# Performance work log

Measured on AMD Instinct MI355X. Metric: run time of the kernel, lower is better.

## Reference

```python
import jax, jax.numpy as jnp
import numpy as np
import math

B, H, S, D = 2, 16, 2048, 128
INV_SCALE = math.sqrt(D)  # divisor applied to QK^T logits (dropout_p = 0.0)


def setup_inputs() -> dict:
    key = jax.random.key(0)
    kq, kk, kv = jax.random.split(key, 3)
    return {
        "query": jax.random.normal(kq, (B, H, S, D), dtype=jnp.float32),
        "key": jax.random.normal(kk, (B, H, S, D), dtype=jnp.float32),
        "value": jax.random.normal(kv, (B, H, S, D), dtype=jnp.float32),
    }


def reference(query, key, value):
    # v1 = Q @ K^T ; v2 = v1 / inv_scale ; v3 = softmax(v2, -1) ; dropout(p=0) is identity ; out = v3 @ V
    scores = jnp.einsum("bhqd,bhkd->bhqk", query, key) / INV_SCALE  # [B,H,Sq,Sk]
    probs = jax.nn.softmax(scores, axis=-1)
    return jnp.einsum("bhqk,bhkd->bhqd", probs, value)  # [B,H,Sq,D]
```

## Files before the change

### kernel.cpp

```cpp
#include <hip/hip_runtime.h>
#include <hip/hip_bf16.h>

typedef __bf16 bf16x8 __attribute__((ext_vector_type(8)));
typedef float f32x4 __attribute__((ext_vector_type(4)));

#define S_LEN 2048
#define D_DIM 128
#define BH 32
#define BN 64
#define NT (S_LEN / BN)
#define NWAVE 8
#define QSCALE (0.08838834764831845f * 1.4426950408889634f)


__global__ __launch_bounds__(512, 4)
void fa_fwd_kernel(const float* __restrict__ Qg, const float* __restrict__ Kg,
                   const float* __restrict__ Vg, float* __restrict__ Og) {
    __shared__ __bf16 Klds[BN][D_DIM + 8];
    __shared__ __bf16 Vlds[D_DIM][BN + 8];
    __shared__ __bf16 Plds[NWAVE][16][BN + 8];

    const int bh   = blockIdx.x & (BH - 1);
    const int qt   = blockIdx.x >> 5;
    const int tid  = threadIdx.x;
    const int wave = tid >> 6;
    const int lane = tid & 63;
    const int quad = lane >> 4;
    const int m16  = lane & 15;

    const float* Qh = Qg + bh * (S_LEN * D_DIM);
    const float* Kh = Kg + bh * (S_LEN * D_DIM);
    const float* Vh = Vg + bh * (S_LEN * D_DIM);
    float*       Oh = Og + bh * (S_LEN * D_DIM);

    const int qrow_base = qt * 128 + wave * 16;

    bf16x8 qf[4];
#pragma unroll
    for (int ks = 0; ks < 4; ++ks) {
        const float* qp = Qh + (qrow_base + m16) * D_DIM + ks * 32 + quad * 8;
        const float4 a = *(const float4*)(qp);
        const float4 b = *(const float4*)(qp + 4);
        bf16x8 f;
        f[0] = (__bf16)(a.x * QSCALE); f[1] = (__bf16)(a.y * QSCALE);
        f[2] = (__bf16)(a.z * QSCALE); f[3] = (__bf16)(a.w * QSCALE);
        f[4] = (__bf16)(b.x * QSCALE); f[5] = (__bf16)(b.y * QSCALE);
        f[6] = (__bf16)(b.z * QSCALE); f[7] = (__bf16)(b.w * QSCALE);
        qf[ks] = f;
    }

    f32x4 o_acc[8];
#pragma unroll
    for (int nt = 0; nt < 8; ++nt) {
        o_acc[nt][0] = 0.f; o_acc[nt][1] = 0.f; o_acc[nt][2] = 0.f; o_acc[nt][3] = 0.f;
    }
    float l_part[4] = {0.f, 0.f, 0.f, 0.f};

    for (int kt = 0; kt < NT; ++kt) {
        __syncthreads();

        {
            const float* kg = Kh + kt * BN * D_DIM;
#pragma unroll
            for (int i = 0; i < 2; ++i) {
                const int idx = tid + i * 512;
                const int r = idx >> 4, c8 = idx & 15;
                const float4 a = *(const float4*)(kg + r * D_DIM + c8 * 8);
                const float4 b = *(const float4*)(kg + r * D_DIM + c8 * 8 + 4);
                bf16x8 w;
                w[0] = (__bf16)a.x; w[1] = (__bf16)a.y; w[2] = (__bf16)a.z; w[3] = (__bf16)a.w;
                w[4] = (__bf16)b.x; w[5] = (__bf16)b.y; w[6] = (__bf16)b.z; w[7] = (__bf16)b.w;
                *(bf16x8*)&Klds[r][c8 * 8] = w;
            }
            const float* vg = Vh + kt * BN * D_DIM;
            const int c4 = tid & 31, rp = tid >> 5;
#pragma unroll
            for (int i = 0; i < 2; ++i) {
                const int r = (rp + i * 16) * 2;
                const float4 v0 = *(const float4*)(vg + r * D_DIM + c4 * 4);
                const float4 v1 = *(const float4*)(vg + (r + 1) * D_DIM + c4 * 4);
                const float* p0 = reinterpret_cast<const float*>(&v0);
                const float* p1 = reinterpret_cast<const float*>(&v1);
                const int kb = r >> 3, jj = r & 7;
#pragma unroll
                for (int j = 0; j < 4; ++j) {
                    const int d = c4 * 4 + j;
                    union { __bf16 h[2]; unsigned int u; } pk;
                    pk.h[0] = (__bf16)p0[j]; pk.h[1] = (__bf16)p1[j];
                    *(unsigned int*)&Vlds[d][((kb ^ ((d >> 3) & 7)) << 3) + jj] = pk.u;
                }
            }
        }
        __syncthreads();

        f32x4 sacc[4];
#pragma unroll
        for (int nt = 0; nt < 4; ++nt) {
            sacc[nt][0] = 0.f; sacc[nt][1] = 0.f; sacc[nt][2] = 0.f; sacc[nt][3] = 0.f;
        }
#pragma unroll
        for (int ks = 0; ks < 4; ++ks)
#pragma unroll
            for (int nt = 0; nt < 4; ++nt) {
                const bf16x8 kf = *(const bf16x8*)&Klds[nt * 16 + m16][ks * 32 + quad * 8];
                sacc[nt] = __builtin_amdgcn_mfma_f32_16x16x32_bf16(qf[ks], kf, sacc[nt], 0, 0, 0);
            }

#pragma unroll
        for (int nt = 0; nt < 4; ++nt)
#pragma unroll
            for (int r = 0; r < 4; ++r) {
                const float p = __builtin_amdgcn_exp2f(sacc[nt][r]);
                l_part[r] += p;
                Plds[wave][quad * 4 + r][nt * 16 + m16] = (__bf16)p;
            }

#pragma unroll
        for (int ks = 0; ks < 2; ++ks) {
            const bf16x8 pa = *(const bf16x8*)&Plds[wave][m16][ks * 32 + quad * 8];
#pragma unroll
            for (int nt = 0; nt < 8; ++nt) {
                const int d = nt * 16 + m16;
                const bf16x8 vf =
                    *(const bf16x8*)&Vlds[d][((ks * 4 + quad) ^ ((d >> 3) & 7)) << 3];
                o_acc[nt] = __builtin_amdgcn_mfma_f32_16x16x32_bf16(pa, vf, o_acc[nt], 0, 0, 0);
            }
        }
    }

#pragma unroll
    for (int xm = 1; xm <= 8; xm <<= 1)
#pragma unroll
        for (int r = 0; r < 4; ++r)
            l_part[r] += __shfl_xor(l_part[r], xm, 64);

    float inv[4];
#pragma unroll
    for (int r = 0; r < 4; ++r) inv[r] = 1.0f / l_part[r];
#pragma unroll
    for (int nt = 0; nt < 8; ++nt)
#pragma unroll
        for (int r = 0; r < 4; ++r)
            Oh[(qrow_base + quad * 4 + r) * D_DIM + nt * 16 + m16] = o_acc[nt][r] * inv[r];
}

extern "C" void kernel_launch(void* const* d_in, const int* in_sizes, int n_in,
                              void* d_out, int out_size, void* d_ws, size_t ws_size,
                              hipStream_t stream) {
    const float* Q = (const float*)d_in[0];
    const float* K = (const float*)d_in[1];
    const float* V = (const float*)d_in[2];
    float* O = (float*)d_out;
    dim3 grid(BH * (S_LEN / 128));
    fa_fwd_kernel<<<grid, 512, 0, stream>>>(Q, K, V, O);
}
```

Before: 223.0 us.

## Register-prefetch next K/V tile and restructure V transpose store with MFMA priority

Global loads of the next K and V tiles are issued into registers right after the LDS barrier, so their latency overlaps the current tile's QK and PV MFMA work. The V transpose is reorganised so each lane loads eight rows of two columns and writes two full bf16x8 vectors to LDS, replacing many 32-bit scattered stores. s_setprio raises wave priority around the MFMA blocks. The cost is extra VGPRs for the staging registers, which may pressure occupancy under the 512x4 launch bounds.

```diff
diff --git a/kernel.cpp b/kernel.cpp
--- a/kernel.cpp
+++ b/kernel.cpp
@@ -56,48 +56,71 @@
     }
     float l_part[4] = {0.f, 0.f, 0.f, 0.f};
 
+    const int krow = tid >> 4;
+    const int kc8  = tid & 15;
+    const int vd0   = lane * 2;
+    const int vrow  = wave * 8;
+    const int vslot = (wave ^ ((vd0 >> 3) & 7)) << 3;
+
+    float4 kreg[4];
+    float2 vreg[8];
+    {
+        const float* kg = Kh;
+        kreg[0] = *(const float4*)(kg + krow * D_DIM + kc8 * 8);
+        kreg[1] = *(const float4*)(kg + krow * D_DIM + kc8 * 8 + 4);
+        kreg[2] = *(const float4*)(kg + (32 + krow) * D_DIM + kc8 * 8);
+        kreg[3] = *(const float4*)(kg + (32 + krow) * D_DIM + kc8 * 8 + 4);
+        const float* vp = Vh + vrow * D_DIM + vd0;
+#pragma unroll
+        for (int kr = 0; kr < 8; ++kr)
+            vreg[kr] = *(const float2*)(vp + kr * D_DIM);
+    }
+
     for (int kt = 0; kt < NT; ++kt) {
         __syncthreads();
 
         {
-            const float* kg = Kh + kt * BN * D_DIM;
+            bf16x8 w;
+            w[0] = (__bf16)kreg[0].x; w[1] = (__bf16)kreg[0].y;
+            w[2] = (__bf16)kreg[0].z; w[3] = (__bf16)kreg[0].w;
+            w[4] = (__bf16)kreg[1].x; w[5] = (__bf16)kreg[1].y;
+            w[6] = (__bf16)kreg[1].z; w[7] = (__bf16)kreg[1].w;
+            *(bf16x8*)&Klds[krow][kc8 * 8] = w;
+            w[0] = (__bf16)kreg[2].x; w[1] = (__bf16)kreg[2].y;
+            w[2] = (__bf16)kreg[2].z; w[3] = (__bf16)kreg[2].w;
+            w[4] = (__bf16)kreg[3].x; w[5] = (__bf16)kreg[3].y;
+            w[6] = (__bf16)kreg[3].z; w[7] = (__bf16)kreg[3].w;
+            *(bf16x8*)&Klds[32 + krow][kc8 * 8] = w;
+
+            bf16x8 w0, w1;
 #pragma unroll
-            for (int i = 0; i < 2; ++i) {
-                const int idx = tid + i * 512;
-                const int r = idx >> 4, c8 = idx & 15;
-                const float4 a = *(const float4*)(kg + r * D_DIM + c8 * 8);
-                const float4 b = *(const float4*)(kg + r * D_DIM + c8 * 8 + 4);
-                bf16x8 w;
-                w[0] = (__bf16)a.x; w[1] = (__bf16)a.y; w[2] = (__bf16)a.z; w[3] = (__bf16)a.w;
-                w[4] = (__bf16)b.x; w[5] = (__bf16)b.y; w[6] = (__bf16)b.z; w[7] = (__bf16)b.w;
-                *(bf16x8*)&Klds[r][c8 * 8] = w;
+            for (int kr = 0; kr < 8; ++kr) {
+                w0[kr] = (__bf16)vreg[kr].x;
+                w1[kr] = (__bf16)vreg[kr].y;
             }
-            const float* vg = Vh + kt * BN * D_DIM;
-            const int c4 = tid & 31, rp = tid >> 5;
-#pragma unroll
-            for (int i = 0; i < 2; ++i) {
-                const int r = (rp + i * 16) * 2;
-                const float4 v0 = *(const float4*)(vg + r * D_DIM + c4 * 4);
-                const float4 v1 = *(const float4*)(vg + (r + 1) * D_DIM + c4 * 4);
-                const float* p0 = reinterpret_cast<const float*>(&v0);
-                const float* p1 = reinterpret_cast<const float*>(&v1);
-                const int kb = r >> 3, jj = r & 7;
-#pragma unroll
-                for (int j = 0; j < 4; ++j) {
-                    const int d = c4 * 4 + j;
-                    union { __bf16 h[2]; unsigned int u; } pk;
-                    pk.h[0] = (__bf16)p0[j]; pk.h[1] = (__bf16)p1[j];
-                    *(unsigned int*)&Vlds[d][((kb ^ ((d >> 3) & 7)) << 3) + jj] = pk.u;
-                }
-            }
+            *(bf16x8*)&Vlds[vd0][vslot]     = w0;
+            *(bf16x8*)&Vlds[vd0 + 1][vslot] = w1;
         }
         __syncthreads();
+
+        if (kt + 1 < NT) {
+            const float* kg = Kh + (kt + 1) * (BN * D_DIM);
+            kreg[0] = *(const float4*)(kg + krow * D_DIM + kc8 * 8);
+            kreg[1] = *(const float4*)(kg + krow * D_DIM + kc8 * 8 + 4);
+            kreg[2] = *(const float4*)(kg + (32 + krow) * D_DIM + kc8 * 8);
+            kreg[3] = *(const float4*)(kg + (32 + krow) * D_DIM + kc8 * 8 + 4);
+            const float* vp = Vh + (kt + 1) * (BN * D_DIM) + vrow * D_DIM + vd0;
+#pragma unroll
+            for (int kr = 0; kr < 8; ++kr)
+                vreg[kr] = *(const float2*)(vp + kr * D_DIM);
+        }
 
         f32x4 sacc[4];
 #pragma unroll
         for (int nt = 0; nt < 4; ++nt) {
             sacc[nt][0] = 0.f; sacc[nt][1] = 0.f; sacc[nt][2] = 0.f; sacc[nt][3] = 0.f;
         }
+        __builtin_amdgcn_s_setprio(1);
 #pragma unroll
         for (int ks = 0; ks < 4; ++ks)
 #pragma unroll
@@ -105,6 +128,7 @@
                 const bf16x8 kf = *(const bf16x8*)&Klds[nt * 16 + m16][ks * 32 + quad * 8];
                 sacc[nt] = __builtin_amdgcn_mfma_f32_16x16x32_bf16(qf[ks], kf, sacc[nt], 0, 0, 0);
             }
+        __builtin_amdgcn_s_setprio(0);
 
 #pragma unroll
         for (int nt = 0; nt < 4; ++nt)
@@ -115,6 +139,7 @@
                 Plds[wave][quad * 4 + r][nt * 16 + m16] = (__bf16)p;
             }
 
+        __builtin_amdgcn_s_setprio(1);
 #pragma unroll
         for (int ks = 0; ks < 2; ++ks) {
             const bf16x8 pa = *(const bf16x8*)&Plds[wave][m16][ks * 32 + quad * 8];
@@ -126,6 +151,7 @@
                 o_acc[nt] = __builtin_amdgcn_mfma_f32_16x16x32_bf16(pa, vf, o_acc[nt], 0, 0, 0);
             }
         }
+        __builtin_amdgcn_s_setprio(0);
     }
 
 #pragma unroll
```

Result: slower. 261.8 us (+17.4%).

## Give each wave two 16-row Q fragments and cut block to four waves

Applied to the files above, without the earlier changes.

Each wave now handles 32 query rows as two MFMA row fragments, so every K and V fragment read from LDS is reused twice. The block shrinks from 512 to 256 threads, and the K/V staging is restructured to issue all global loads first, then convert and store. The V transpose now writes whole bf16x8 vectors instead of packed pairs. s_setprio raises wave priority around the MFMA sections, while the extra accumulators add register pressure and occupancy may drop.

```diff
diff --git a/kernel.cpp b/kernel.cpp
--- a/kernel.cpp
+++ b/kernel.cpp
@@ -9,16 +9,16 @@
 #define BH 32
 #define BN 64
 #define NT (S_LEN / BN)
-#define NWAVE 8
+#define NWAVE 4
 #define QSCALE (0.08838834764831845f * 1.4426950408889634f)
 
 
-__global__ __launch_bounds__(512, 4)
+__global__ __launch_bounds__(256, 2)
 void fa_fwd_kernel(const float* __restrict__ Qg, const float* __restrict__ Kg,
                    const float* __restrict__ Vg, float* __restrict__ Og) {
     __shared__ __bf16 Klds[BN][D_DIM + 8];
     __shared__ __bf16 Vlds[D_DIM][BN + 8];
-    __shared__ __bf16 Plds[NWAVE][16][BN + 8];
+    __shared__ __bf16 Plds[NWAVE][32][BN + 8];
 
     const int bh   = blockIdx.x & (BH - 1);
     const int qt   = blockIdx.x >> 5;
@@ -33,115 +33,149 @@
     const float* Vh = Vg + bh * (S_LEN * D_DIM);
     float*       Oh = Og + bh * (S_LEN * D_DIM);
 
-    const int qrow_base = qt * 128 + wave * 16;
+    const int qrow_base = qt * 128 + wave * 32;
 
-    bf16x8 qf[4];
+    bf16x8 qf[2][4];
 #pragma unroll
-    for (int ks = 0; ks < 4; ++ks) {
-        const float* qp = Qh + (qrow_base + m16) * D_DIM + ks * 32 + quad * 8;
-        const float4 a = *(const float4*)(qp);
-        const float4 b = *(const float4*)(qp + 4);
-        bf16x8 f;
-        f[0] = (__bf16)(a.x * QSCALE); f[1] = (__bf16)(a.y * QSCALE);
-        f[2] = (__bf16)(a.z * QSCALE); f[3] = (__bf16)(a.w * QSCALE);
-        f[4] = (__bf16)(b.x * QSCALE); f[5] = (__bf16)(b.y * QSCALE);
-        f[6] = (__bf16)(b.z * QSCALE); f[7] = (__bf16)(b.w * QSCALE);
-        qf[ks] = f;
-    }
+    for (int mf = 0; mf < 2; ++mf)
+#pragma unroll
+        for (int ks = 0; ks < 4; ++ks) {
+            const float* qp = Qh + (qrow_base + mf * 16 + m16) * D_DIM + ks * 32 + quad * 8;
+            const float4 a = *(const float4*)(qp);
+            const float4 b = *(const float4*)(qp + 4);
+            bf16x8 f;
+            f[0] = (__bf16)(a.x * QSCALE); f[1] = (__bf16)(a.y * QSCALE);
+            f[2] = (__bf16)(a.z * QSCALE); f[3] = (__bf16)(a.w * QSCALE);
+            f[4] = (__bf16)(b.x * QSCALE); f[5] = (__bf16)(b.y * QSCALE);
+            f[6] = (__bf16)(b.z * QSCALE); f[7] = (__bf16)(b.w * QSCALE);
+            qf[mf][ks] = f;
+        }
 
-    f32x4 o_acc[8];
+    f32x4 o_acc[2][8];
 #pragma unroll
-    for (int nt = 0; nt < 8; ++nt) {
-        o_acc[nt][0] = 0.f; o_acc[nt][1] = 0.f; o_acc[nt][2] = 0.f; o_acc[nt][3] = 0.f;
-    }
-    float l_part[4] = {0.f, 0.f, 0.f, 0.f};
+    for (int mf = 0; mf < 2; ++mf)
+#pragma unroll
+        for (int nt = 0; nt < 8; ++nt) {
+            o_acc[mf][nt][0] = 0.f; o_acc[mf][nt][1] = 0.f;
+            o_acc[mf][nt][2] = 0.f; o_acc[mf][nt][3] = 0.f;
+        }
+    float l_part[2][4] = {{0.f, 0.f, 0.f, 0.f}, {0.f, 0.f, 0.f, 0.f}};
+
+    const int krow = tid >> 4;
+    const int kc8  = tid & 15;
+    const int vd0   = (tid & 31) * 4;
+    const int vgrp  = tid >> 5;
+    const int vslot = (vgrp ^ ((vd0 >> 3) & 7)) << 3;
 
     for (int kt = 0; kt < NT; ++kt) {
         __syncthreads();
 
+        float4 vreg[8];
         {
-            const float* kg = Kh + kt * BN * D_DIM;
+            const float* vp = Vh + kt * (BN * D_DIM) + vgrp * 8 * D_DIM + vd0;
 #pragma unroll
-            for (int i = 0; i < 2; ++i) {
-                const int idx = tid + i * 512;
-                const int r = idx >> 4, c8 = idx & 15;
-                const float4 a = *(const float4*)(kg + r * D_DIM + c8 * 8);
-                const float4 b = *(const float4*)(kg + r * D_DIM + c8 * 8 + 4);
-                bf16x8 w;
-                w[0] = (__bf16)a.x; w[1] = (__bf16)a.y; w[2] = (__bf16)a.z; w[3] = (__bf16)a.w;
-                w[4] = (__bf16)b.x; w[5] = (__bf16)b.y; w[6] = (__bf16)b.z; w[7] = (__bf16)b.w;
-                *(bf16x8*)&Klds[r][c8 * 8] = w;
+            for (int kr = 0; kr < 8; ++kr)
+                vreg[kr] = *(const float4*)(vp + kr * D_DIM);
+        }
+        float4 kreg[8];
+        {
+            const float* kg = Kh + kt * (BN * D_DIM);
+#pragma unroll
+            for (int i = 0; i < 4; ++i) {
+                kreg[2 * i]     = *(const float4*)(kg + (krow + 16 * i) * D_DIM + kc8 * 8);
+                kreg[2 * i + 1] = *(const float4*)(kg + (krow + 16 * i) * D_DIM + kc8 * 8 + 4);
             }
-            const float* vg = Vh + kt * BN * D_DIM;
-            const int c4 = tid & 31, rp = tid >> 5;
+        }
+
 #pragma unroll
-            for (int i = 0; i < 2; ++i) {
-                const int r = (rp + i * 16) * 2;
-                const float4 v0 = *(const float4*)(vg + r * D_DIM + c4 * 4);
-                const float4 v1 = *(const float4*)(vg + (r + 1) * D_DIM + c4 * 4);
-                const float* p0 = reinterpret_cast<const float*>(&v0);
-                const float* p1 = reinterpret_cast<const float*>(&v1);
-                const int kb = r >> 3, jj = r & 7;
+        for (int i = 0; i < 4; ++i) {
+            bf16x8 w;
+            w[0] = (__bf16)kreg[2 * i].x;     w[1] = (__bf16)kreg[2 * i].y;
+            w[2] = (__bf16)kreg[2 * i].z;     w[3] = (__bf16)kreg[2 * i].w;
+            w[4] = (__bf16)kreg[2 * i + 1].x; w[5] = (__bf16)kreg[2 * i + 1].y;
+            w[6] = (__bf16)kreg[2 * i + 1].z; w[7] = (__bf16)kreg[2 * i + 1].w;
+            *(bf16x8*)&Klds[krow + 16 * i][kc8 * 8] = w;
+        }
+
 #pragma unroll
-                for (int j = 0; j < 4; ++j) {
-                    const int d = c4 * 4 + j;
-                    union { __bf16 h[2]; unsigned int u; } pk;
-                    pk.h[0] = (__bf16)p0[j]; pk.h[1] = (__bf16)p1[j];
-                    *(unsigned int*)&Vlds[d][((kb ^ ((d >> 3) & 7)) << 3) + jj] = pk.u;
-                }
+        for (int j = 0; j < 4; ++j) {
+            bf16x8 w;
+#pragma unroll
+            for (int kr = 0; kr < 8; ++kr) {
+                const float* pv = reinterpret_cast<const float*>(&vreg[kr]);
+                w[kr] = (__bf16)pv[j];
             }
+            *(bf16x8*)&Vlds[vd0 + j][vslot] = w;
         }
         __syncthreads();
 
-        f32x4 sacc[4];
+        f32x4 sacc[2][4];
 #pragma unroll
-        for (int nt = 0; nt < 4; ++nt) {
-            sacc[nt][0] = 0.f; sacc[nt][1] = 0.f; sacc[nt][2] = 0.f; sacc[nt][3] = 0.f;
-        }
+        for (int mf = 0; mf < 2; ++mf)
+#pragma unroll
+            for (int nt = 0; nt < 4; ++nt) {
+                sacc[mf][nt][0] = 0.f; sacc[mf][nt][1] = 0.f;
+                sacc[mf][nt][2] = 0.f; sacc[mf][nt][3] = 0.f;
+            }
+        __builtin_amdgcn_s_setprio(1);
 #pragma unroll
         for (int ks = 0; ks < 4; ++ks)
 #pragma unroll
             for (int nt = 0; nt < 4; ++nt) {
                 const bf16x8 kf = *(const bf16x8*)&Klds[nt * 16 + m16][ks * 32 + quad * 8];
-                sacc[nt] = __builtin_amdgcn_mfma_f32_16x16x32_bf16(qf[ks], kf, sacc[nt], 0, 0, 0);
+                sacc[0][nt] = __builtin_amdgcn_mfma_f32_16x16x32_bf16(qf[0][ks], kf, sacc[0][nt], 0, 0, 0);
+                sacc[1][nt] = __builtin_amdgcn_mfma_f32_16x16x32_bf16(qf[1][ks], kf, sacc[1][nt], 0, 0, 0);
             }
+        __builtin_amdgcn_s_setprio(0);
 
 #pragma unroll
-        for (int nt = 0; nt < 4; ++nt)
+        for (int mf = 0; mf < 2; ++mf)
 #pragma unroll
-            for (int r = 0; r < 4; ++r) {
-                const float p = __builtin_amdgcn_exp2f(sacc[nt][r]);
-                l_part[r] += p;
-                Plds[wave][quad * 4 + r][nt * 16 + m16] = (__bf16)p;
-            }
+            for (int nt = 0; nt < 4; ++nt)
+#pragma unroll
+                for (int r = 0; r < 4; ++r) {
+                    const float p = __builtin_amdgcn_exp2f(sacc[mf][nt][r]);
+                    l_part[mf][r] += p;
+                    Plds[wave][mf * 16 + quad * 4 + r][nt * 16 + m16] = (__bf16)p;
+                }
 
+        __builtin_amdgcn_s_setprio(1);
 #pragma unroll
         for (int ks = 0; ks < 2; ++ks) {
-            const bf16x8 pa = *(const bf16x8*)&Plds[wave][m16][ks * 32 + quad * 8];
+            const bf16x8 pa0 = *(const bf16x8*)&Plds[wave][m16]     [ks * 32 + quad * 8];
+            const bf16x8 pa1 = *(const bf16x8*)&Plds[wave][16 + m16][ks * 32 + quad * 8];
 #pragma unroll
             for (int nt = 0; nt < 8; ++nt) {
                 const int d = nt * 16 + m16;
                 const bf16x8 vf =
                     *(const bf16x8*)&Vlds[d][((ks * 4 + quad) ^ ((d >> 3) & 7)) << 3];
-                o_acc[nt] = __builtin_amdgcn_mfma_f32_16x16x32_bf16(pa, vf, o_acc[nt], 0, 0, 0);
+                o_acc[0][nt] = __builtin_amdgcn_mfma_f32_16x16x32_bf16(pa0, vf, o_acc[0][nt], 0, 0, 0);
+                o_acc[1][nt] = __builtin_amdgcn_mfma_f32_16x16x32_bf16(pa1, vf, o_acc[1][nt], 0, 0, 0);
             }
         }
+        __builtin_amdgcn_s_setprio(0);
     }
 
 #pragma unroll
     for (int xm = 1; xm <= 8; xm <<= 1)
 #pragma unroll
-        for (int r = 0; r < 4; ++r)
-            l_part[r] += __shfl_xor(l_part[r], xm, 64);
+        for (int mf = 0; mf < 2; ++mf)
+#pragma unroll
+            for (int r = 0; r < 4; ++r)
+                l_part[mf][r] += __shfl_xor(l_part[mf][r], xm, 64);
 
-    float inv[4];
 #pragma unroll
-    for (int r = 0; r < 4; ++r) inv[r] = 1.0f / l_part[r];
+    for (int mf = 0; mf < 2; ++mf) {
+        float inv[4];
 #pragma unroll
-    for (int nt = 0; nt < 8; ++nt)
+        for (int r = 0; r < 4; ++r) inv[r] = 1.0f / l_part[mf][r];
 #pragma unroll
-        for (int r = 0; r < 4; ++r)
-            Oh[(qrow_base + quad * 4 + r) * D_DIM + nt * 16 + m16] = o_acc[nt][r] * inv[r];
+        for (int nt = 0; nt < 8; ++nt)
+#pragma unroll
+            for (int r = 0; r < 4; ++r)
+                Oh[(qrow_base + mf * 16 + quad * 4 + r) * D_DIM + nt * 16 + m16] =
+                    o_acc[mf][nt][r] * inv[r];
+    }
 }
 
 extern "C" void kernel_launch(void* const* d_in, const int* in_sizes, int n_in,
@@ -152,5 +186,5 @@
     const float* V = (const float*)d_in[2];
     float* O = (float*)d_out;
     dim3 grid(BH * (S_LEN / 128));
-    fa_fwd_kernel<<<grid, 512, 0, stream>>>(Q, K, V, O);
+    fa_fwd_kernel<<<grid, 256, 0, stream>>>(Q, K, V, O);
 }
```

Result: faster. 212.3 us (-4.8%).
